# Optimization experiments

Hardware: AMD Instinct MI355X
Metric: run time of the kernel (lower is better)

The kernel has to match this reference:

```python
import jax, jax.numpy as jnp
import numpy as np

V = 32000; D = 256; H = 8; L = 2; FF = 1024; S = 512; B = 32
M = 4096          # mem_max_entries
NC = 10           # num_classes
K = 4             # retrieve top-k
TH = 0.5          # write threshold
EPS = 1e-8


def setup_inputs() -> dict:
    key = jax.random.key(0)
    ks = jax.random.split(key, 24)
    s = 0.02
    def nrm(k, shape):
        return jax.random.normal(k, shape, jnp.float32) * s
    return {
        "input_ids": jax.random.randint(ks[0], (B, S), 0, V),
        "tok_emb": nrm(ks[1], (V, D)),
        "pos_emb": nrm(ks[2], (S, D)),
        # per-layer params stacked on leading dim L
        "Wqkv": nrm(ks[3], (L, 3 * D, D)), "bqkv": jnp.zeros((L, 3 * D)),
        "Wo": nrm(ks[4], (L, D, D)), "bo": jnp.zeros((L, D)),
        "ln1_g": jnp.ones((L, D)), "ln1_b": jnp.zeros((L, D)),
        "W1": nrm(ks[5], (L, FF, D)), "b1": jnp.zeros((L, FF)),
        "W2": nrm(ks[6], (L, D, FF)), "b2": jnp.zeros((L, D)),
        "ln2_g": jnp.ones((L, D)), "ln2_b": jnp.zeros((L, D)),
        # write gate MLP (d -> d -> 1, sigmoid)
        "Wg1": nrm(ks[7], (D, D)), "bg1": jnp.zeros((D,)),
        "Wg2": nrm(ks[8], (1, D)), "bg2": jnp.zeros((1,)),
        # classifier
        "Wc": nrm(ks[9], (NC, D)), "bc": jnp.zeros((NC,)),
    }


def _layer_norm(x, g, b):
    m = x.mean(-1, keepdims=True)
    v = ((x - m) ** 2).mean(-1, keepdims=True)
    return (x - m) / jnp.sqrt(v + 1e-5) * g + b


def _encoder_layer(x, Wqkv, bqkv, Wo, bo, g1, b1, W1, bf1, W2, bf2, g2, b2):
    # post-LN TransformerEncoderLayer, relu activation, batch_first
    Bx, Sx, Dx = x.shape
    dh = Dx // H
    qkv = x @ Wqkv.T + bqkv                     # [B,S,3D]
    q, k, v = jnp.split(qkv, 3, axis=-1)
    def heads(t):
        return t.reshape(Bx, Sx, H, dh).transpose(0, 2, 1, 3)  # [B,H,S,dh]
    q, k, v = heads(q), heads(k), heads(v)
    scores = jnp.einsum("bhqd,bhkd->bhqk", q, k) / jnp.sqrt(jnp.float32(dh))
    attn = jax.nn.softmax(scores, axis=-1)
    o = jnp.einsum("bhqk,bhkd->bhqd", attn, v)
    o = o.transpose(0, 2, 1, 3).reshape(Bx, Sx, Dx)
    o = o @ Wo.T + bo
    x = _layer_norm(x + o, g1, b1)
    ff = jax.nn.relu(x @ W1.T + bf1) @ W2.T + bf2
    return _layer_norm(x + ff, g2, b2)


def reference(input_ids, tok_emb, pos_emb, Wqkv, bqkv, Wo, bo, ln1_g, ln1_b,
              W1, b1, W2, b2, ln2_g, ln2_b, Wg1, bg1, Wg2, bg2, Wc, bc):
    Bx, Sx = input_ids.shape
    x = tok_emb[input_ids] + pos_emb[jnp.arange(Sx)][None, :, :]
    for l in range(L):
        x = _encoder_layer(x, Wqkv[l], bqkv[l], Wo[l], bo[l], ln1_g[l], ln1_b[l],
                           W1[l], b1[l], W2[l], b2[l], ln2_g[l], ln2_b[l])
    h = x                                        # [B,S,D]
    cls_state = h[:, 0, :]                       # [B,D]

    # --- write gate: per-token store into external memory (capped FIFO scatter) ---
    flat_h = h.reshape(-1, D)                    # [B*S, D]
    probs = jax.nn.sigmoid(jax.nn.relu(flat_h @ Wg1.T + bg1) @ Wg2.T + bg2)[:, 0]
    mask = probs > TH                            # [B*S]
    slot = jnp.cumsum(mask.astype(jnp.int32)) - 1
    valid = mask & (slot < M)
    idx = jnp.where(valid, slot, M)              # overflow -> dummy row M
    mem = jnp.zeros((M + 1, D), jnp.float32).at[idx].set(flat_h)[:M]
    count = jnp.minimum(mask.sum(), M)
    occupied = jnp.arange(M) < count             # [M]

    # --- top-k cosine retrieval with CLS as query ---
    qn = cls_state / (jnp.linalg.norm(cls_state, axis=-1, keepdims=True) + EPS)
    kn = mem / (jnp.linalg.norm(mem, axis=-1, keepdims=True) + EPS)
    sims = qn @ kn.T                             # [B,M]
    sims = jnp.where(occupied[None, :], sims, -1e9)
    top_sims, top_idx = jax.lax.top_k(sims, K)   # [B,K]
    vals = mem[top_idx]                          # [B,K,D] (unoccupied rows are zero)
    attn = jax.nn.softmax(top_sims, axis=-1)
    mem_vec = jnp.einsum("bk,bkd->bd", attn, vals)
    mem_vec = jnp.where(count > 0, mem_vec, 0.0)

    cls_aug = cls_state + mem_vec
    return cls_aug @ Wc.T + bc                   # [B,NC]
```

## Files before the change

kernel.cpp:

```cpp
#include <hip/hip_runtime.h>
#include <math.h>

#define D_   256
#define H_   8
#define L_   2
#define FF_  1024
#define S_   512
#define B_   32
#define M_   4096
#define NC_  10
#define ROWS (B_*S_)

typedef __attribute__((ext_vector_type(8))) short bf16x8;
typedef __attribute__((ext_vector_type(4))) float f32x4;
typedef unsigned int uint32;
typedef unsigned short ushort16;

__device__ __forceinline__ float wave_sum(float v) {
#pragma unroll
  for (int off = 1; off < 64; off <<= 1) v += __shfl_xor(v, off, 64);
  return v;
}

__device__ __forceinline__ unsigned short bf16_rne(float x) {
  unsigned int b = __float_as_uint(x);
  return (unsigned short)((b + 0x7FFFu + ((b >> 16) & 1u)) >> 16);
}
__device__ __forceinline__ float bf16_f(unsigned short h) {
  return __uint_as_float(((unsigned int)h) << 16);
}
__device__ __forceinline__ uint32 pack_split(float x) {
  const unsigned short h = bf16_rne(x);
  const unsigned short l = bf16_rne(x - bf16_f(h));
  return (uint32)h | ((uint32)l << 16);
}
__device__ __forceinline__ void unpack_store(unsigned short* Hq, unsigned short* Lq,
                                             int off, uint4 v) {
  uint2 hp, lp;
  hp.x = (v.x & 0xffffu) | (v.y << 16);
  hp.y = (v.z & 0xffffu) | (v.w << 16);
  lp.x = (v.x >> 16) | (v.y & 0xffff0000u);
  lp.y = (v.z >> 16) | (v.w & 0xffff0000u);
  *(uint2*)&Hq[off] = hp;
  *(uint2*)&Lq[off] = lp;
}
__device__ __forceinline__ bf16x8 ld_frag(const unsigned short* p, int off) {
  union { uint2 u[2]; bf16x8 v; } x;
  x.u[0] = *(const uint2*)(p + off);
  x.u[1] = *(const uint2*)(p + off + 4);
  return x.v;
}

__global__ __launch_bounds__(256) void pack_f32(const float* __restrict__ src,
                                                uint32* __restrict__ dst, int n4) {
  const int i = blockIdx.x * 256 + threadIdx.x;
  if (i < n4) {
    const float4 v = ((const float4*)src)[i];
    uint4 o;
    o.x = pack_split(v.x); o.y = pack_split(v.y);
    o.z = pack_split(v.z); o.w = pack_split(v.w);
    ((uint4*)dst)[i] = o;
  }
}

__global__ __launch_bounds__(256) void emb_kernel(const int* __restrict__ ids,
                                                  const float* __restrict__ tok,
                                                  const float* __restrict__ pos,
                                                  float* __restrict__ x,
                                                  uint32* __restrict__ xp) {
  const int row  = blockIdx.x * 4 + (threadIdx.x >> 6);
  const int lane = threadIdx.x & 63;
  const int id = ids[row];
  const int s  = row & (S_ - 1);
  const float4 t = *(const float4*)(tok + (size_t)id * D_ + lane * 4);
  const float4 p = *(const float4*)(pos + (size_t)s  * D_ + lane * 4);
  float4 r; r.x = t.x + p.x; r.y = t.y + p.y; r.z = t.z + p.z; r.w = t.w + p.w;
  *(float4*)(x + (size_t)row * D_ + lane * 4) = r;
  uint4 o;
  o.x = pack_split(r.x); o.y = pack_split(r.y);
  o.z = pack_split(r.z); o.w = pack_split(r.w);
  *(uint4*)(xp + (size_t)row * D_ + lane * 4) = o;
}

#define LP 36
template<int BM, int RELU, int PACKOUT>
__global__ __launch_bounds__(512, 4) void gemm_mfma(const uint32* __restrict__ Ap,
                                                    const uint32* __restrict__ Bp,
                                                    const float* __restrict__ bias,
                                                    float* __restrict__ C,
                                                    uint32* __restrict__ Cp,
                                                    int M, int N, int K, int NX) {
  constexpr int WGM = BM / 64;
  constexpr int WGN = 8 / WGM;
  constexpr int WN  = 128 / WGN;
  constexpr int FN  = WN / 16;
  __shared__ __align__(16) unsigned short Ah[BM * LP];
  __shared__ __align__(16) unsigned short Al[BM * LP];
  __shared__ __align__(16) unsigned short Bh[128 * LP];
  __shared__ __align__(16) unsigned short Bl[128 * LP];

  const int q8 = gridDim.x >> 3;
  const int orig = (blockIdx.x & 7) * q8 + (blockIdx.x >> 3);
  const int by = orig / NX, bx = orig % NX;

  const int tid  = threadIdx.x;
  const int lane = tid & 63;
  const int wid  = tid >> 6;
  const int wm = wid / WGN, wn = wid % WGN;
  const int m0 = by * BM, n0 = bx * 128;
  const int lrow  = lane & 15;
  const int khalf = (lane >> 4) * 8;

  const int srow = tid >> 3;
  const int kq   = (tid & 7) << 2;
  const uint32* Aptr = Ap + (size_t)(m0 + srow) * K + kq;
  const uint32* Bptr = Bp + (size_t)(n0 + srow) * K + kq;

  f32x4 acc[4][FN];
#pragma unroll
  for (int i = 0; i < 4; i++)
#pragma unroll
    for (int j = 0; j < FN; j++) acc[i][j] = (f32x4){0.f, 0.f, 0.f, 0.f};

  uint4 pa[BM / 64], pb[2];
#pragma unroll
  for (int j = 0; j < BM / 64; j++) pa[j] = *(const uint4*)(Aptr + (size_t)j * 64 * K);
#pragma unroll
  for (int j = 0; j < 2; j++) pb[j] = *(const uint4*)(Bptr + (size_t)j * 64 * K);

  for (int k0 = 0; k0 < K; k0 += 32) {
    const int kn = (k0 + 32 < K) ? (k0 + 32) : k0;
    uint4 na[BM / 64], nb[2];
#pragma unroll
    for (int j = 0; j < BM / 64; j++) na[j] = *(const uint4*)(Aptr + (size_t)j * 64 * K + kn);
#pragma unroll
    for (int j = 0; j < 2; j++) nb[j] = *(const uint4*)(Bptr + (size_t)j * 64 * K + kn);

    __syncthreads();
#pragma unroll
    for (int j = 0; j < BM / 64; j++)
      unpack_store(Ah, Al, (srow + j * 64) * LP + kq, pa[j]);
#pragma unroll
    for (int j = 0; j < 2; j++)
      unpack_store(Bh, Bl, (srow + j * 64) * LP + kq, pb[j]);
    __syncthreads();

    bf16x8 ah[4], al[4], bh[FN], bl[FN];
#pragma unroll
    for (int fm = 0; fm < 4; fm++) {
      const int r = (wm * 64 + fm * 16 + lrow) * LP + khalf;
      ah[fm] = ld_frag(Ah, r);
      al[fm] = ld_frag(Al, r);
    }
#pragma unroll
    for (int fn = 0; fn < FN; fn++) {
      const int r = (wn * WN + fn * 16 + lrow) * LP + khalf;
      bh[fn] = ld_frag(Bh, r);
      bl[fn] = ld_frag(Bl, r);
    }
#pragma unroll
    for (int fm = 0; fm < 4; fm++)
#pragma unroll
      for (int fn = 0; fn < FN; fn++) {
        acc[fm][fn] = __builtin_amdgcn_mfma_f32_16x16x32_bf16(ah[fm], bh[fn], acc[fm][fn], 0, 0, 0);
        acc[fm][fn] = __builtin_amdgcn_mfma_f32_16x16x32_bf16(ah[fm], bl[fn], acc[fm][fn], 0, 0, 0);
        acc[fm][fn] = __builtin_amdgcn_mfma_f32_16x16x32_bf16(al[fm], bh[fn], acc[fm][fn], 0, 0, 0);
      }
#pragma unroll
    for (int j = 0; j < BM / 64; j++) pa[j] = na[j];
#pragma unroll
    for (int j = 0; j < 2; j++) pb[j] = nb[j];
  }

#pragma unroll
  for (int fm = 0; fm < 4; fm++)
#pragma unroll
    for (int fn = 0; fn < FN; fn++) {
      const int mrow = m0 + wm * 64 + fm * 16 + (lane >> 4) * 4;
      const int ncol = n0 + wn * WN + fn * 16 + (lane & 15);
      const float bi = bias[ncol];
#pragma unroll
      for (int r = 0; r < 4; r++) {
        float v = acc[fm][fn][r] + bi;
        if (RELU) v = fmaxf(v, 0.f);
        if (PACKOUT) Cp[(size_t)(mrow + r) * N + ncol] = pack_split(v);
        else         C[(size_t)(mrow + r) * N + ncol] = v;
      }
    }
}

#define KP 36
#define VP 516
__global__ __launch_bounds__(1024, 4) void attn_mfma(const uint32* __restrict__ qkv,
                                                     uint32* __restrict__ o) {
  __shared__ __align__(16) unsigned short Kh[512 * KP];
  __shared__ __align__(16) unsigned short Kl[512 * KP];
  __shared__ __align__(16) unsigned short Vth[32 * VP];
  __shared__ __align__(16) unsigned short Vtl[32 * VP];

  const int q8g = gridDim.x >> 3;
  const int obh = (blockIdx.x & 7) * q8g + (blockIdx.x >> 3);
  const int b = obh >> 3, h = obh & 7;
  const int tid = threadIdx.x;
  const int lane = tid & 63;
  const int wv = tid >> 6;
  const uint32* base = qkv + (size_t)b * (S_ * 768) + h * 32;

  if (tid < 512) {
    const int slot = tid;
    const int s5 = slot & 31;
    const int orig = (slot & ~31) + 8 * ((s5 >> 2) & 3) + ((s5 >> 4) << 2) + (s5 & 3);
    const uint32* p = base + (size_t)orig * 768 + 256;
#pragma unroll
    for (int j = 0; j < 8; j++)
      unpack_store(Kh, Kl, slot * KP + j * 4, *(const uint4*)(p + j * 4));
  } else {
    const int u  = tid - 512;
    const int kp = u & 255;
    const int dg = (u >> 8) * 16;
    const uint32* p0 = base + (size_t)(2 * kp) * 768 + 512 + dg;
    const uint32* p1 = p0 + 768;
    union { uint4 u4[4]; uint32 w[16]; } a0, a1;
#pragma unroll
    for (int i = 0; i < 4; i++) {
      a0.u4[i] = *(const uint4*)(p0 + i * 4);
      a1.u4[i] = *(const uint4*)(p1 + i * 4);
    }
#pragma unroll
    for (int d = 0; d < 16; d++) {
      const uint32 w0 = a0.w[d], w1 = a1.w[d];
      *(uint32*)&Vth[(dg + d) * VP + 2 * kp] = (w0 & 0xffffu) | (w1 << 16);
      *(uint32*)&Vtl[(dg + d) * VP + 2 * kp] = (w0 >> 16) | (w1 & 0xffff0000u);
    }
  }

  const int q0 = wv * 32;
  bf16x8 qh[2], ql[2];
#pragma unroll
  for (int f = 0; f < 2; f++) {
    const uint32* qp = base + (size_t)(q0 + f * 16 + (lane & 15)) * 768 + ((lane >> 4) * 8);
    union { uint4 u4[2]; uint32 w[8]; } qu;
    qu.u4[0] = *(const uint4*)qp;
    qu.u4[1] = *(const uint4*)(qp + 4);
    bf16x8 vh, vl;
#pragma unroll
    for (int j = 0; j < 8; j++) {
      const uint32 p = qu.w[j];
      const float qf = __uint_as_float(p << 16) + __uint_as_float(p & 0xffff0000u);
      const float sv = qf * 0.17677669529663687f;
      const unsigned short hh = bf16_rne(sv);
      vh[j] = (short)hh;
      vl[j] = (short)bf16_rne(sv - bf16_f(hh));
    }
    qh[f] = vh; ql[f] = vl;
  }

  __syncthreads();

  f32x4 oacc[2][2];
#pragma unroll
  for (int i = 0; i < 2; i++)
#pragma unroll
    for (int j = 0; j < 2; j++) oacc[i][j] = (f32x4){0.f, 0.f, 0.f, 0.f};
  float lacc[2] = {0.f, 0.f};

  for (int kt = 0; kt < S_; kt += 32) {
    bf16x8 kah[2], kal[2];
#pragma unroll
    for (int u = 0; u < 2; u++) {
      const int off = (kt + u * 16 + (lane & 15)) * KP + ((lane >> 4) * 8);
      kah[u] = ld_frag(Kh, off);
      kal[u] = ld_frag(Kl, off);
    }
    bf16x8 vah[2], val[2];
#pragma unroll
    for (int df = 0; df < 2; df++) {
      const int off = (df * 16 + (lane & 15)) * VP + kt + ((lane >> 4) * 8);
      vah[df] = ld_frag(Vth, off);
      val[df] = ld_frag(Vtl, off);
    }
    f32x4 s[2][2];
#pragma unroll
    for (int u = 0; u < 2; u++)
#pragma unroll
      for (int f = 0; f < 2; f++) {
        f32x4 a = (f32x4){0.f, 0.f, 0.f, 0.f};
        a = __builtin_amdgcn_mfma_f32_16x16x32_bf16(kal[u], qh[f], a, 0, 0, 0);
        a = __builtin_amdgcn_mfma_f32_16x16x32_bf16(kah[u], ql[f], a, 0, 0, 0);
        a = __builtin_amdgcn_mfma_f32_16x16x32_bf16(kah[u], qh[f], a, 0, 0, 0);
        s[u][f] = a;
      }
#pragma unroll
    for (int f = 0; f < 2; f++) {
      union { uint32 w[4]; bf16x8 v; } ph, pl;
#pragma unroll
      for (int u = 0; u < 2; u++) {
        const float p0 = __expf(s[u][f][0]);
        const float p1 = __expf(s[u][f][1]);
        const float p2 = __expf(s[u][f][2]);
        const float p3 = __expf(s[u][f][3]);
        lacc[f] += (p0 + p1) + (p2 + p3);
        unsigned int h01, h23;
        asm volatile("v_cvt_pk_bf16_f32 %0, %1, %2" : "=v"(h01) : "v"(p0), "v"(p1));
        asm volatile("v_cvt_pk_bf16_f32 %0, %1, %2" : "=v"(h23) : "v"(p2), "v"(p3));
        const float r0 = p0 - __uint_as_float(h01 << 16);
        const float r1 = p1 - __uint_as_float(h01 & 0xffff0000u);
        const float r2 = p2 - __uint_as_float(h23 << 16);
        const float r3 = p3 - __uint_as_float(h23 & 0xffff0000u);
        unsigned int l01, l23;
        asm volatile("v_cvt_pk_bf16_f32 %0, %1, %2" : "=v"(l01) : "v"(r0), "v"(r1));
        asm volatile("v_cvt_pk_bf16_f32 %0, %1, %2" : "=v"(l23) : "v"(r2), "v"(r3));
        ph.w[u * 2 + 0] = h01;
        ph.w[u * 2 + 1] = h23;
        pl.w[u * 2 + 0] = l01;
        pl.w[u * 2 + 1] = l23;
      }
#pragma unroll
      for (int df = 0; df < 2; df++) {
        oacc[df][f] = __builtin_amdgcn_mfma_f32_16x16x32_bf16(val[df], ph.v, oacc[df][f], 0, 0, 0);
        oacc[df][f] = __builtin_amdgcn_mfma_f32_16x16x32_bf16(vah[df], pl.v, oacc[df][f], 0, 0, 0);
        oacc[df][f] = __builtin_amdgcn_mfma_f32_16x16x32_bf16(vah[df], ph.v, oacc[df][f], 0, 0, 0);
      }
    }
  }

#pragma unroll
  for (int f = 0; f < 2; f++) {
    lacc[f] += __shfl_xor(lacc[f], 16, 64);
    lacc[f] += __shfl_xor(lacc[f], 32, 64);
  }
#pragma unroll
  for (int f = 0; f < 2; f++) {
    const float inv = 1.f / lacc[f];
    const int q = q0 + f * 16 + (lane & 15);
    uint32* op = o + (size_t)(b * S_ + q) * D_ + h * 32;
#pragma unroll
    for (int df = 0; df < 2; df++) {
      const int dbase = df * 16 + (lane >> 4) * 4;
#pragma unroll
      for (int r = 0; r < 4; r++)
        op[dbase + r] = pack_split(oacc[df][f][r] * inv);
    }
  }
}

__global__ __launch_bounds__(256) void add_ln(const float* __restrict__ x,
                                              const float* __restrict__ y,
                                              const float* __restrict__ g,
                                              const float* __restrict__ bta,
                                              float* __restrict__ out,
                                              uint32* __restrict__ outp) {
  const int row  = blockIdx.x * 4 + (threadIdx.x >> 6);
  const int lane = threadIdx.x & 63;
  const size_t base = (size_t)row * D_ + lane * 4;
  const float4 xv = *(const float4*)(x + base);
  const float4 yv = *(const float4*)(y + base);
  float v[4] = {xv.x + yv.x, xv.y + yv.y, xv.z + yv.z, xv.w + yv.w};
  float s = v[0] + v[1] + v[2] + v[3];
  s = wave_sum(s);
  const float mean = s * (1.f / 256.f);
  float d[4] = {v[0] - mean, v[1] - mean, v[2] - mean, v[3] - mean};
  float sq = d[0] * d[0] + d[1] * d[1] + d[2] * d[2] + d[3] * d[3];
  sq = wave_sum(sq);
  const float inv = 1.f / sqrtf(sq * (1.f / 256.f) + 1e-5f);
  const float4 gv = *(const float4*)(g + lane * 4);
  const float4 bv = *(const float4*)(bta + lane * 4);
  float4 r;
  r.x = d[0] * inv * gv.x + bv.x; r.y = d[1] * inv * gv.y + bv.y;
  r.z = d[2] * inv * gv.z + bv.z; r.w = d[3] * inv * gv.w + bv.w;
  *(float4*)(out + base) = r;
  uint4 o;
  o.x = pack_split(r.x); o.y = pack_split(r.y);
  o.z = pack_split(r.z); o.w = pack_split(r.w);
  *(uint4*)(outp + base) = o;
}

__global__ __launch_bounds__(256) void gate_mask(const float* __restrict__ t,
                                                 const float* __restrict__ Wg2,
                                                 const float* __restrict__ bg2,
                                                 int* __restrict__ mask) {
  const int row  = blockIdx.x * 4 + (threadIdx.x >> 6);
  const int lane = threadIdx.x & 63;
  const float4 tv = *(const float4*)(t + (size_t)row * D_ + lane * 4);
  const float4 wv = *(const float4*)(Wg2 + lane * 4);
  float s = tv.x * wv.x + tv.y * wv.y + tv.z * wv.z + tv.w * wv.w;
  s = wave_sum(s);
  if (lane == 0) mask[row] = (s + bg2[0]) > 0.f ? 1 : 0;
}

__global__ __launch_bounds__(256) void scan_kernel(const int* __restrict__ mask,
                                                   int* __restrict__ slots,
                                                   int* __restrict__ countp) {
  __shared__ int wtot[4];
  const int tid = threadIdx.x;
  const int lane = tid & 63, wid = tid >> 6;
  const int base = tid * 64;
  int s = 0;
#pragma unroll 8
  for (int i = 0; i < 64; i++) s += mask[base + i];
  int inc = s;
#pragma unroll
  for (int off = 1; off < 64; off <<= 1) {
    const int t = __shfl_up(inc, off, 64);
    if (lane >= off) inc += t;
  }
  if (lane == 63) wtot[wid] = inc;
  __syncthreads();
  int woff = 0;
#pragma unroll
  for (int w = 0; w < 4; w++) woff += (w < wid) ? wtot[w] : 0;
  const int total = wtot[0] + wtot[1] + wtot[2] + wtot[3];
  if (tid == 0) countp[0] = total < M_ ? total : M_;
  int run = woff + inc - s;
  for (int i = 0; i < 64; i++) {
    const int r = base + i;
    const int mk = mask[r];
    slots[r] = (mk && run < M_) ? run : -1;
    run += mk;
  }
}

__global__ __launch_bounds__(256) void scatter_kernel(const float* __restrict__ h,
                                                      const int* __restrict__ slots,
                                                      float* __restrict__ mem) {
  const int row  = blockIdx.x * 4 + (threadIdx.x >> 6);
  const int lane = threadIdx.x & 63;
  const int sl = slots[row];
  if (sl >= 0)
    *(float4*)(mem + (size_t)sl * D_ + lane * 4) =
        *(const float4*)(h + (size_t)row * D_ + lane * 4);
}

__global__ __launch_bounds__(256) void qnorm_kernel(const float* __restrict__ h,
                                                    float* __restrict__ qden) {
  const int b    = blockIdx.x * 4 + (threadIdx.x >> 6);
  const int lane = threadIdx.x & 63;
  const float4 c = *(const float4*)(h + (size_t)b * S_ * D_ + lane * 4);
  float sq = c.x * c.x + c.y * c.y + c.z * c.z + c.w * c.w;
  sq = wave_sum(sq);
  if (lane == 0) qden[b] = sqrtf(sq) + 1e-8f;
}

__global__ __launch_bounds__(256) void sims_kernel(const float* __restrict__ h,
                                                   const float* __restrict__ mem,
                                                   const float* __restrict__ qden,
                                                   const int* __restrict__ countp,
                                                   float* __restrict__ sims) {
  __shared__ float cls[B_ * D_];
  __shared__ float qd[B_];
  const int tid = threadIdx.x;
  const int lane = tid & 63, wid = tid >> 6;
  for (int i = tid; i < B_ * D_ / 4; i += 256) {
    const int flat = i * 4;
    const int b = flat >> 8, d = flat & 255;
    *(float4*)&cls[flat] = *(const float4*)(h + (size_t)b * S_ * D_ + d);
  }
  if (tid < B_) qd[tid] = qden[tid];
  __syncthreads();
  const int count = countp[0];
  const int r = blockIdx.x * 4 + wid;
  const float4 m4 = *(const float4*)(mem + (size_t)r * D_ + lane * 4);
  float sq = m4.x * m4.x + m4.y * m4.y + m4.z * m4.z + m4.w * m4.w;
  sq = wave_sum(sq);
  const float rn = sqrtf(sq) + 1e-8f;
  if (r < count) {
    for (int b = 0; b < B_; b++) {
      const float4 c4 = *(const float4*)&cls[b * D_ + lane * 4];
      float dt = m4.x * c4.x + m4.y * c4.y + m4.z * c4.z + m4.w * c4.w;
      dt = wave_sum(dt);
      if (lane == 0) sims[b * M_ + r] = dt / (qd[b] * rn);
    }
  } else if (lane == 0) {
    for (int b = 0; b < B_; b++) sims[b * M_ + r] = -1e9f;
  }
}

__global__ __launch_bounds__(256) void topk_mix(const float* __restrict__ h,
                                                const float* __restrict__ mem,
                                                const float* __restrict__ simsg,
                                                const int* __restrict__ countp,
                                                const float* __restrict__ Wc,
                                                const float* __restrict__ bc,
                                                float* __restrict__ out) {
  __shared__ float sims[M_];
  __shared__ float cls[D_];
  __shared__ float wv4[4];
  __shared__ int   wi4[4];
  __shared__ float aug[D_];
  __shared__ float tv[4];
  __shared__ int   tix[4];

  const int b = blockIdx.x, tid = threadIdx.x;
  const int lane = tid & 63, wid = tid >> 6;
  const int count = countp[0];

  for (int i = tid; i < M_; i += 256) sims[i] = simsg[b * M_ + i];
  cls[tid] = h[(size_t)b * S_ * D_ + tid];
  __syncthreads();

  for (int k = 0; k < 4; k++) {
    float bv = -INFINITY; int bi = 1 << 30;
#pragma unroll
    for (int rr = 0; rr < M_ / 256; rr++) {
      const int r = tid + rr * 256;
      const float v = sims[r];
      if (v > bv || (v == bv && r < bi)) { bv = v; bi = r; }
    }
#pragma unroll
    for (int off = 1; off < 64; off <<= 1) {
      const float ov = __shfl_xor(bv, off, 64);
      const int   oi = __shfl_xor(bi, off, 64);
      if (ov > bv || (ov == bv && oi < bi)) { bv = ov; bi = oi; }
    }
    if (lane == 0) { wv4[wid] = bv; wi4[wid] = bi; }
    __syncthreads();
    if (tid == 0) {
      float bb = wv4[0]; int bbi = wi4[0];
#pragma unroll
      for (int i = 1; i < 4; i++)
        if (wv4[i] > bb || (wv4[i] == bb && wi4[i] < bbi)) { bb = wv4[i]; bbi = wi4[i]; }
      tv[k] = bb; tix[k] = bbi; sims[bbi] = -INFINITY;
    }
    __syncthreads();
  }

  float w[4];
  {
    const float mx = tv[0];
    float ws = 0.f;
#pragma unroll
    for (int k = 0; k < 4; k++) { w[k] = expf(tv[k] - mx); ws += w[k]; }
    const float inv = 1.f / ws;
#pragma unroll
    for (int k = 0; k < 4; k++) w[k] *= inv;
  }

  {
    float mv = 0.f;
    if (count > 0) {
#pragma unroll
      for (int k = 0; k < 4; k++) mv = fmaf(w[k], mem[(size_t)tix[k] * D_ + tid], mv);
    }
    aug[tid] = cls[tid] + mv;
  }
  __syncthreads();

  const float4 a4 = *(const float4*)&aug[lane * 4];
  for (int c = wid; c < NC_; c += 4) {
    const float4 wc = *(const float4*)(Wc + (size_t)c * D_ + lane * 4);
    float dt = a4.x * wc.x + a4.y * wc.y + a4.z * wc.z + a4.w * wc.w;
    dt = wave_sum(dt);
    if (lane == 0) out[b * NC_ + c] = dt + bc[c];
  }
}

extern "C" void kernel_launch(void* const* d_in, const int* in_sizes, int n_in,
                              void* d_out, int out_size, void* d_ws, size_t ws_size,
                              hipStream_t stream) {
  const int*   ids  = (const int*)d_in[0];
  const float* tok  = (const float*)d_in[1];
  const float* pos  = (const float*)d_in[2];
  const float* Wqkv = (const float*)d_in[3];
  const float* bqkv = (const float*)d_in[4];
  const float* Wo   = (const float*)d_in[5];
  const float* bo   = (const float*)d_in[6];
  const float* ln1g = (const float*)d_in[7];
  const float* ln1b = (const float*)d_in[8];
  const float* W1   = (const float*)d_in[9];
  const float* b1   = (const float*)d_in[10];
  const float* W2   = (const float*)d_in[11];
  const float* b2   = (const float*)d_in[12];
  const float* ln2g = (const float*)d_in[13];
  const float* ln2b = (const float*)d_in[14];
  const float* Wg1  = (const float*)d_in[15];
  const float* bg1  = (const float*)d_in[16];
  const float* Wg2  = (const float*)d_in[17];
  const float* bg2  = (const float*)d_in[18];
  const float* Wc   = (const float*)d_in[19];
  const float* bc   = (const float*)d_in[20];
  float* out = (float*)d_out;

  float*  xA    = (float*)d_ws;
  float*  xB    = xA  + (size_t)ROWS * D_;
  float*  pb    = xB  + (size_t)ROWS * D_;
  uint32* xAp   = (uint32*)(pb + (size_t)ROWS * D_);
  uint32* xBp   = xAp + (size_t)ROWS * D_;
  uint32* obp   = xBp + (size_t)ROWS * D_;
  uint32* bigp  = obp + (size_t)ROWS * D_;
  uint32* Wqkvp = bigp + (size_t)ROWS * FF_;
  uint32* Wop   = Wqkvp + (size_t)L_ * 768 * 256;
  uint32* W1p   = Wop   + (size_t)L_ * 256 * 256;
  uint32* W2p   = W1p   + (size_t)L_ * 1024 * 256;
  uint32* Wg1p  = W2p   + (size_t)L_ * 256 * 1024;
  float*  mem   = (float*)(Wg1p + 256 * 256);
  float*  qden  = mem + (size_t)M_ * D_;
  float*  sims  = qden + 64;
  int*    mask  = (int*)(sims + (size_t)B_ * M_);
  int*    slots = mask + ROWS;
  int*    cnt   = slots + ROWS;

  pack_f32<<<(L_ * 768 * 256 / 4 + 255) / 256, 256, 0, stream>>>(Wqkv, Wqkvp, L_ * 768 * 256 / 4);
  pack_f32<<<(L_ * 256 * 256 / 4 + 255) / 256, 256, 0, stream>>>(Wo, Wop, L_ * 256 * 256 / 4);
  pack_f32<<<(L_ * 1024 * 256 / 4 + 255) / 256, 256, 0, stream>>>(W1, W1p, L_ * 1024 * 256 / 4);
  pack_f32<<<(L_ * 256 * 1024 / 4 + 255) / 256, 256, 0, stream>>>(W2, W2p, L_ * 256 * 1024 / 4);
  pack_f32<<<(256 * 256 / 4 + 255) / 256, 256, 0, stream>>>(Wg1, Wg1p, 256 * 256 / 4);

  emb_kernel<<<ROWS / 4, 256, 0, stream>>>(ids, tok, pos, xA, xAp);

  for (int l = 0; l < L_; l++) {
    gemm_mfma<128, 0, 1><<<768, 512, 0, stream>>>(
        xAp, Wqkvp + (size_t)l * 768 * 256, bqkv + l * 768, nullptr, bigp, ROWS, 768, 256, 6);
    attn_mfma<<<B_ * H_, 1024, 0, stream>>>(bigp, obp);
    gemm_mfma<64, 0, 0><<<512, 512, 0, stream>>>(
        obp, Wop + (size_t)l * 256 * 256, bo + l * 256, pb, nullptr, ROWS, 256, 256, 2);
    add_ln<<<ROWS / 4, 256, 0, stream>>>(xA, pb, ln1g + l * 256, ln1b + l * 256, xB, xBp);
    gemm_mfma<128, 1, 1><<<1024, 512, 0, stream>>>(
        xBp, W1p + (size_t)l * 1024 * 256, b1 + l * 1024, nullptr, bigp, ROWS, 1024, 256, 8);
    gemm_mfma<64, 0, 0><<<512, 512, 0, stream>>>(
        bigp, W2p + (size_t)l * 256 * 1024, b2 + l * 256, pb, nullptr, ROWS, 256, 1024, 2);
    add_ln<<<ROWS / 4, 256, 0, stream>>>(xB, pb, ln2g + l * 256, ln2b + l * 256, xA, xAp);
  }

  gemm_mfma<64, 1, 0><<<512, 512, 0, stream>>>(
      xAp, Wg1p, bg1, pb, nullptr, ROWS, 256, 256, 2);
  gate_mask<<<ROWS / 4, 256, 0, stream>>>(pb, Wg2, bg2, mask);
  scan_kernel<<<1, 256, 0, stream>>>(mask, slots, cnt);
  (void)hipMemsetAsync(mem, 0, (size_t)M_ * D_ * sizeof(float), stream);
  scatter_kernel<<<ROWS / 4, 256, 0, stream>>>(xA, slots, mem);

  qnorm_kernel<<<B_ / 4, 256, 0, stream>>>(xA, qden);
  sims_kernel<<<M_ / 4, 256, 0, stream>>>(xA, mem, qden, cnt, sims);
  topk_mix<<<B_, 256, 0, stream>>>(xA, mem, sims, cnt, Wc, bc, out);
}
```

Before: 455.4 us.

## Fuse N=256 GEMMs with residual LayerNorm and gate-mask epilogues

Adds a gemm_ln kernel where each 1024-thread block computes a full 64x256 output tile, so row-wise reductions can run in the epilogue. The out-projection and FFN2 GEMMs now fold in bias, residual add and LayerNorm, and the gate GEMM folds in ReLU, the Wg2 dot product and thresholding. This drops the separate add_ln and gate_mask launches and the fp32 intermediate buffer round trip through global memory. In exchange it uses one-pass variance (E[x^2]-mean^2), writes the output with strided scalar stores instead of vectorized ones, and uses a different tile shape that may lower MFMA efficiency or occupancy.

```diff
diff --git a/kernel.cpp b/kernel.cpp
--- a/kernel.cpp
+++ b/kernel.cpp
@@ -14,7 +14,6 @@
 typedef __attribute__((ext_vector_type(8))) short bf16x8;
 typedef __attribute__((ext_vector_type(4))) float f32x4;
 typedef unsigned int uint32;
-typedef unsigned short ushort16;
 
 __device__ __forceinline__ float wave_sum(float v) {
 #pragma unroll
@@ -187,6 +186,182 @@
         else         C[(size_t)(mrow + r) * N + ncol] = v;
       }
     }
+}
+
+template<int MODE>
+__global__ __launch_bounds__(1024, 2) void gemm_ln(const uint32* __restrict__ Ap,
+                                                   const uint32* __restrict__ Bp,
+                                                   const float* __restrict__ bias,
+                                                   const float* __restrict__ resid,
+                                                   const float* __restrict__ g,
+                                                   const float* __restrict__ beta,
+                                                   const float* __restrict__ Wg2,
+                                                   const float* __restrict__ bg2,
+                                                   float* __restrict__ outF,
+                                                   uint32* __restrict__ outP,
+                                                   int* __restrict__ mask,
+                                                   int K) {
+  __shared__ __align__(16) unsigned short Ah[64 * LP];
+  __shared__ __align__(16) unsigned short Al[64 * LP];
+  __shared__ __align__(16) unsigned short Bh[256 * LP];
+  __shared__ __align__(16) unsigned short Bl[256 * LP];
+  __shared__ float psumS[8][64];
+  __shared__ float psumQ[8][64];
+  __shared__ float meanL[64];
+  __shared__ float invL[64];
+
+  const int q8 = gridDim.x >> 3;
+  const int m0 = ((blockIdx.x & 7) * q8 + (blockIdx.x >> 3)) * 64;
+
+  const int tid  = threadIdx.x;
+  const int lane = tid & 63;
+  const int wid  = tid >> 6;
+  const int wm = wid >> 3, wn = wid & 7;
+  const int lrow  = lane & 15;
+  const int khalf = (lane >> 4) * 8;
+
+  const int srow = tid >> 3;
+  const int kq   = (tid & 7) << 2;
+  const uint32* Aptr = Ap + (size_t)(m0 + srow) * K + kq;
+  const uint32* Bptr = Bp + (size_t)srow * K + kq;
+
+  f32x4 acc[2][2];
+#pragma unroll
+  for (int i = 0; i < 2; i++)
+#pragma unroll
+    for (int j = 0; j < 2; j++) acc[i][j] = (f32x4){0.f, 0.f, 0.f, 0.f};
+
+  uint4 pa, pb0, pb1;
+  if (tid < 512) pa = *(const uint4*)Aptr;
+  pb0 = *(const uint4*)Bptr;
+  pb1 = *(const uint4*)(Bptr + (size_t)128 * K);
+
+  for (int k0 = 0; k0 < K; k0 += 32) {
+    const int kn = (k0 + 32 < K) ? (k0 + 32) : k0;
+    uint4 na, nb0, nb1;
+    if (tid < 512) na = *(const uint4*)(Aptr + kn);
+    nb0 = *(const uint4*)(Bptr + kn);
+    nb1 = *(const uint4*)(Bptr + (size_t)128 * K + kn);
+
+    __syncthreads();
+    if (tid < 512) unpack_store(Ah, Al, srow * LP + kq, pa);
+    unpack_store(Bh, Bl, srow * LP + kq, pb0);
+    unpack_store(Bh, Bl, (srow + 128) * LP + kq, pb1);
+    __syncthreads();
+
+    bf16x8 ah[2], al[2], bh[2], bl[2];
+#pragma unroll
+    for (int fm = 0; fm < 2; fm++) {
+      const int r = (wm * 32 + fm * 16 + lrow) * LP + khalf;
+      ah[fm] = ld_frag(Ah, r);
+      al[fm] = ld_frag(Al, r);
+    }
+#pragma unroll
+    for (int fn = 0; fn < 2; fn++) {
+      const int r = (wn * 32 + fn * 16 + lrow) * LP + khalf;
+      bh[fn] = ld_frag(Bh, r);
+      bl[fn] = ld_frag(Bl, r);
+    }
+#pragma unroll
+    for (int fm = 0; fm < 2; fm++)
+#pragma unroll
+      for (int fn = 0; fn < 2; fn++) {
+        acc[fm][fn] = __builtin_amdgcn_mfma_f32_16x16x32_bf16(ah[fm], bh[fn], acc[fm][fn], 0, 0, 0);
+        acc[fm][fn] = __builtin_amdgcn_mfma_f32_16x16x32_bf16(ah[fm], bl[fn], acc[fm][fn], 0, 0, 0);
+        acc[fm][fn] = __builtin_amdgcn_mfma_f32_16x16x32_bf16(al[fm], bh[fn], acc[fm][fn], 0, 0, 0);
+      }
+    pa = na; pb0 = nb0; pb1 = nb1;
+  }
+
+  const int c0 = wn * 32 + (lane & 15);
+  const int c1 = c0 + 16;
+  const float b0 = bias[c0], b1 = bias[c1];
+
+  float vv[2][2][4];
+  float rs[2][4], rq[2][4];
+
+  if (MODE == 0) {
+#pragma unroll
+    for (int fm = 0; fm < 2; fm++)
+#pragma unroll
+      for (int r = 0; r < 4; r++) {
+        const int row = m0 + wm * 32 + fm * 16 + (lane >> 4) * 4 + r;
+        const float x0 = resid[(size_t)row * 256 + c0];
+        const float x1 = resid[(size_t)row * 256 + c1];
+        const float a = acc[fm][0][r] + b0 + x0;
+        const float b = acc[fm][1][r] + b1 + x1;
+        vv[fm][0][r] = a; vv[fm][1][r] = b;
+        rs[fm][r] = a + b;
+        rq[fm][r] = a * a + b * b;
+      }
+  } else {
+    const float w0 = Wg2[c0], w1 = Wg2[c1];
+#pragma unroll
+    for (int fm = 0; fm < 2; fm++)
+#pragma unroll
+      for (int r = 0; r < 4; r++) {
+        const float a = fmaxf(acc[fm][0][r] + b0, 0.f);
+        const float b = fmaxf(acc[fm][1][r] + b1, 0.f);
+        rs[fm][r] = a * w0 + b * w1;
+      }
+  }
+
+#pragma unroll
+  for (int off = 1; off < 16; off <<= 1) {
+#pragma unroll
+    for (int fm = 0; fm < 2; fm++)
+#pragma unroll
+      for (int r = 0; r < 4; r++) {
+        rs[fm][r] += __shfl_xor(rs[fm][r], off, 64);
+        if (MODE == 0) rq[fm][r] += __shfl_xor(rq[fm][r], off, 64);
+      }
+  }
+  if ((lane & 15) == 0) {
+#pragma unroll
+    for (int fm = 0; fm < 2; fm++)
+#pragma unroll
+      for (int r = 0; r < 4; r++) {
+        const int rloc = wm * 32 + fm * 16 + (lane >> 4) * 4 + r;
+        psumS[wn][rloc] = rs[fm][r];
+        if (MODE == 0) psumQ[wn][rloc] = rq[fm][r];
+      }
+  }
+  __syncthreads();
+  if (tid < 64) {
+    float s = 0.f, q = 0.f;
+#pragma unroll
+    for (int w = 0; w < 8; w++) {
+      s += psumS[w][tid];
+      if (MODE == 0) q += psumQ[w][tid];
+    }
+    if (MODE == 0) {
+      const float mean = s * (1.f / 256.f);
+      const float var = q * (1.f / 256.f) - mean * mean;
+      meanL[tid] = mean;
+      invL[tid] = rsqrtf(var + 1e-5f);
+    } else {
+      mask[m0 + tid] = (s + bg2[0]) > 0.f ? 1 : 0;
+    }
+  }
+  if (MODE == 0) {
+    __syncthreads();
+    const float g0 = g[c0], g1 = g[c1];
+    const float be0 = beta[c0], be1 = beta[c1];
+#pragma unroll
+    for (int fm = 0; fm < 2; fm++)
+#pragma unroll
+      for (int r = 0; r < 4; r++) {
+        const int rloc = wm * 32 + fm * 16 + (lane >> 4) * 4 + r;
+        const int row = m0 + rloc;
+        const float mu = meanL[rloc], iv = invL[rloc];
+        const float y0 = (vv[fm][0][r] - mu) * iv * g0 + be0;
+        const float y1 = (vv[fm][1][r] - mu) * iv * g1 + be1;
+        outF[(size_t)row * 256 + c0] = y0;
+        outF[(size_t)row * 256 + c1] = y1;
+        outP[(size_t)row * 256 + c0] = pack_split(y0);
+        outP[(size_t)row * 256 + c1] = pack_split(y1);
+      }
+  }
 }
 
 #define KP 36
@@ -342,50 +517,6 @@
         op[dbase + r] = pack_split(oacc[df][f][r] * inv);
     }
   }
-}
-
-__global__ __launch_bounds__(256) void add_ln(const float* __restrict__ x,
-                                              const float* __restrict__ y,
-                                              const float* __restrict__ g,
-                                              const float* __restrict__ bta,
-                                              float* __restrict__ out,
-                                              uint32* __restrict__ outp) {
-  const int row  = blockIdx.x * 4 + (threadIdx.x >> 6);
-  const int lane = threadIdx.x & 63;
-  const size_t base = (size_t)row * D_ + lane * 4;
-  const float4 xv = *(const float4*)(x + base);
-  const float4 yv = *(const float4*)(y + base);
-  float v[4] = {xv.x + yv.x, xv.y + yv.y, xv.z + yv.z, xv.w + yv.w};
-  float s = v[0] + v[1] + v[2] + v[3];
-  s = wave_sum(s);
-  const float mean = s * (1.f / 256.f);
-  float d[4] = {v[0] - mean, v[1] - mean, v[2] - mean, v[3] - mean};
-  float sq = d[0] * d[0] + d[1] * d[1] + d[2] * d[2] + d[3] * d[3];
-  sq = wave_sum(sq);
-  const float inv = 1.f / sqrtf(sq * (1.f / 256.f) + 1e-5f);
-  const float4 gv = *(const float4*)(g + lane * 4);
-  const float4 bv = *(const float4*)(bta + lane * 4);
-  float4 r;
-  r.x = d[0] * inv * gv.x + bv.x; r.y = d[1] * inv * gv.y + bv.y;
-  r.z = d[2] * inv * gv.z + bv.z; r.w = d[3] * inv * gv.w + bv.w;
-  *(float4*)(out + base) = r;
-  uint4 o;
-  o.x = pack_split(r.x); o.y = pack_split(r.y);
-  o.z = pack_split(r.z); o.w = pack_split(r.w);
-  *(uint4*)(outp + base) = o;
-}
-
-__global__ __launch_bounds__(256) void gate_mask(const float* __restrict__ t,
-                                                 const float* __restrict__ Wg2,
-                                                 const float* __restrict__ bg2,
-                                                 int* __restrict__ mask) {
-  const int row  = blockIdx.x * 4 + (threadIdx.x >> 6);
-  const int lane = threadIdx.x & 63;
-  const float4 tv = *(const float4*)(t + (size_t)row * D_ + lane * 4);
-  const float4 wv = *(const float4*)(Wg2 + lane * 4);
-  float s = tv.x * wv.x + tv.y * wv.y + tv.z * wv.z + tv.w * wv.w;
-  s = wave_sum(s);
-  if (lane == 0) mask[row] = (s + bg2[0]) > 0.f ? 1 : 0;
 }
 
 __global__ __launch_bounds__(256) void scan_kernel(const int* __restrict__ mask,
@@ -582,8 +713,7 @@
 
   float*  xA    = (float*)d_ws;
   float*  xB    = xA  + (size_t)ROWS * D_;
-  float*  pb    = xB  + (size_t)ROWS * D_;
-  uint32* xAp   = (uint32*)(pb + (size_t)ROWS * D_);
+  uint32* xAp   = (uint32*)(xB + (size_t)ROWS * D_);
   uint32* xBp   = xAp + (size_t)ROWS * D_;
   uint32* obp   = xBp + (size_t)ROWS * D_;
   uint32* bigp  = obp + (size_t)ROWS * D_;
@@ -611,19 +741,18 @@
     gemm_mfma<128, 0, 1><<<768, 512, 0, stream>>>(
         xAp, Wqkvp + (size_t)l * 768 * 256, bqkv + l * 768, nullptr, bigp, ROWS, 768, 256, 6);
     attn_mfma<<<B_ * H_, 1024, 0, stream>>>(bigp, obp);
-    gemm_mfma<64, 0, 0><<<512, 512, 0, stream>>>(
-        obp, Wop + (size_t)l * 256 * 256, bo + l * 256, pb, nullptr, ROWS, 256, 256, 2);
-    add_ln<<<ROWS / 4, 256, 0, stream>>>(xA, pb, ln1g + l * 256, ln1b + l * 256, xB, xBp);
+    gemm_ln<0><<<ROWS / 64, 1024, 0, stream>>>(
+        obp, Wop + (size_t)l * 256 * 256, bo + l * 256, xA,
+        ln1g + l * 256, ln1b + l * 256, nullptr, nullptr, xB, xBp, nullptr, 256);
     gemm_mfma<128, 1, 1><<<1024, 512, 0, stream>>>(
         xBp, W1p + (size_t)l * 1024 * 256, b1 + l * 1024, nullptr, bigp, ROWS, 1024, 256, 8);
-    gemm_mfma<64, 0, 0><<<512, 512, 0, stream>>>(
-        bigp, W2p + (size_t)l * 256 * 1024, b2 + l * 256, pb, nullptr, ROWS, 256, 1024, 2);
-    add_ln<<<ROWS / 4, 256, 0, stream>>>(xB, pb, ln2g + l * 256, ln2b + l * 256, xA, xAp);
-  }
-
-  gemm_mfma<64, 1, 0><<<512, 512, 0, stream>>>(
-      xAp, Wg1p, bg1, pb, nullptr, ROWS, 256, 256, 2);
-  gate_mask<<<ROWS / 4, 256, 0, stream>>>(pb, Wg2, bg2, mask);
+    gemm_ln<0><<<ROWS / 64, 1024, 0, stream>>>(
+        bigp, W2p + (size_t)l * 256 * 1024, b2 + l * 256, xB,
+        ln2g + l * 256, ln2b + l * 256, nullptr, nullptr, xA, xAp, nullptr, 1024);
+  }
+
+  gemm_ln<1><<<ROWS / 64, 1024, 0, stream>>>(
+      xAp, Wg1p, bg1, nullptr, nullptr, nullptr, Wg2, bg2, nullptr, nullptr, mask, 256);
   scan_kernel<<<1, 256, 0, stream>>>(mask, slots, cnt);
   (void)hipMemsetAsync(mem, 0, (size_t)M_ * D_ * sizeof(float), stream);
   scatter_kernel<<<ROWS / 4, 256, 0, stream>>>(xA, slots, mem);
```

After: 423.4 us. 7.0% less time.
